# Kernel optimization log

Measured on AMD Instinct MI355X. Metric: run time of the kernel, lower is better.

## Reference

```python
import jax, jax.numpy as jnp
import numpy as np

HID = 15
H = 4
N = 1048576
XD, YD, ZD, TD = 16, 8, 8, 4


def _lin(x, W, b):
    # plain constrained linear (non_negative=False)
    return x @ W.T + b


def _lin_nn(x, W, b):
    # non_negative=True: softplus on the weight before the matmul
    return x @ jax.nn.softplus(W).T + b


def setup_inputs() -> dict:
    key = jax.random.key(0)
    ks = iter(jax.random.split(key, 64))

    def w(shape):
        return jax.random.normal(next(ks), shape, dtype=jnp.float32) * 0.1

    inp = {
        "x0": jax.random.normal(next(ks), (N, XD), dtype=jnp.float32),
        "y0": jax.random.normal(next(ks), (N, YD), dtype=jnp.float32),
        "z0": jax.random.normal(next(ks), (N, ZD), dtype=jnp.float32),
        "t0": jax.random.normal(next(ks), (N, TD), dtype=jnp.float32),
        # y / z / t towers: first layer maps from input dim, rest HIDxHID
        "yW0": w((HID, YD)), "yWs": w((H - 1, HID, HID)), "yb": jnp.zeros((H, HID)),
        "zW0": w((HID, ZD)), "zWs": w((H - 1, HID, HID)), "zb": jnp.zeros((H, HID)),
        "tW0": w((HID, TD)), "tWs": w((H - 1, HID, HID)), "tb": jnp.zeros((H, HID)),
        # first x block (4-branch sum)
        "x0W": w((HID, XD)), "x0b": jnp.zeros((HID,)),
        "y0W": w((HID, YD)), "y0b": jnp.zeros((HID,)),
        "z0W": w((HID, ZD)), "z0b": jnp.zeros((HID,)),
        "t0W": w((HID, TD)), "t0b": jnp.zeros((HID,)),
        # H-1 iterations of 5-branch blocks (stacked along axis 0)
        "xWs": w((H - 1, HID, HID)), "xb": jnp.zeros((H - 1, HID)),
        "xsW": w((H - 1, HID, XD)), "xsb": jnp.zeros((H - 1, HID)),
        "xyW": w((H - 1, HID, HID)), "xyb": jnp.zeros((H - 1, HID)),
        "xzW": w((H - 1, HID, HID)), "xzb": jnp.zeros((H - 1, HID)),
        "xtW": w((H - 1, HID, HID)), "xtb": jnp.zeros((H - 1, HID)),
        "fW": w((HID, HID)), "fb": jnp.zeros((HID,)),
    }
    return inp


def reference(x0, y0, z0, t0,
              yW0, yWs, yb, zW0, zWs, zb, tW0, tWs, tb,
              x0W, x0b, y0W, y0b, z0W, z0b, t0W, t0b,
              xWs, xb, xsW, xsb, xyW, xyb, xzW, xzb, xtW, xtb,
              fW, fb):
    # y tower: softplus activation, non-negative weights
    y = jax.nn.softplus(_lin_nn(y0, yW0, yb[0]))
    for i in range(H - 1):
        y = jax.nn.softplus(_lin_nn(y, yWs[i], yb[i + 1]))
    # z tower: sigmoid activation, unconstrained weights
    z = jax.nn.sigmoid(_lin(z0, zW0, zb[0]))
    for i in range(H - 1):
        z = jax.nn.sigmoid(_lin(z, zWs[i], zb[i + 1]))
    # t tower: sigmoid activation, non-negative weights
    t = jax.nn.sigmoid(_lin_nn(t0, tW0, tb[0]))
    for i in range(H - 1):
        t = jax.nn.sigmoid(_lin_nn(t, tWs[i], tb[i + 1]))
    # x path: multi-branch sums + softplus
    x = _lin(x0, x0W, x0b) + _lin_nn(y0, y0W, y0b) + _lin(z0, z0W, z0b) + _lin_nn(t0, t0W, t0b)
    x = jax.nn.softplus(x)
    for i in range(H - 1):
        x = (_lin_nn(x, xWs[i], xb[i]) + _lin(x0, xsW[i], xsb[i])
             + _lin_nn(y, xyW[i], xyb[i]) + _lin(z, xzW[i], xzb[i])
             + _lin_nn(t, xtW[i], xtb[i]))
        x = jax.nn.softplus(x)
    return _lin(x, fW, fb)
```

## Files before the change

kernel.cpp:

```cpp
#include <hip/hip_runtime.h>
#include <hip/hip_bf16.h>

typedef short s8v  __attribute__((ext_vector_type(8)));
typedef float f32x4 __attribute__((ext_vector_type(4)));
typedef unsigned int u32;
typedef u32 u32x4 __attribute__((ext_vector_type(4)));

#define NSLOT 31
#define NBIAS 17

__device__ __forceinline__ unsigned short b16hi(float v) {
  unsigned int u = __float_as_uint(v);
  return (unsigned short)((u + 0x7FFFu + ((u >> 16) & 1u)) >> 16);
}
__device__ __forceinline__ float b16tof(unsigned short h) {
  return __uint_as_float(((unsigned int)h) << 16);
}
__device__ __forceinline__ unsigned short lobits(float w) {
  return b16hi(w - b16tof(b16hi(w)));
}
__device__ __forceinline__ float sp_stable(float v) {
  float ax = __builtin_fabsf(v);
  float e  = __expf(-ax);
  return fmaxf(v, 0.0f) + __logf(1.0f + e);
}

struct P {
  const float *yW0,*yWs,*yb,*zW0,*zWs,*zb,*tW0,*tWs,*tb;
  const float *x0W,*x0b,*y0W,*y0b,*z0W,*z0b,*t0W,*t0b;
  const float *xWs,*xb,*xsW,*xsb,*xyW,*xyb,*xzW,*xzb,*xtW,*xtb,*fW,*fb;
};

__device__ unsigned short pat15(const float* W, int k, int j, int sp) {
  if (k < 15)           { float v = W[j*15+k];      return b16hi(sp ? sp_stable(v) : v); }
  if (k >= 16 && k < 31){ float v = W[j*15+(k-16)]; return lobits(sp ? sp_stable(v) : v); }
  return 0;
}

__device__ unsigned short wA(int s, int k, int j, const P& p) {
  if (j > 14) return 0;
  if (s == 0) {
    if (k < 8)   return b16hi(sp_stable(p.yW0[j*8+k]));
    if (k < 16)  return lobits(sp_stable(p.yW0[j*8+(k-8)]));
    return 0;
  }
  if (s <= 3)  return pat15(p.yWs + (s-1)*225, k, j, 1);
  if (s == 4) {
    if (k < 8)   return b16hi(p.zW0[j*8+k]);
    if (k < 16)  return lobits(p.zW0[j*8+(k-8)]);
    return 0;
  }
  if (s <= 7)  return pat15(p.zWs + (s-5)*225, k, j, 0);
  if (s == 8) {
    if (k < 4)   return b16hi(sp_stable(p.tW0[j*4+k]));
    if (k < 8)   return lobits(sp_stable(p.tW0[j*4+(k-4)]));
    return 0;
  }
  if (s <= 11) return pat15(p.tWs + (s-9)*225, k, j, 1);
  if (s == 12) {
    if (k < 16) return b16hi(p.x0W[j*16+k]);
    return lobits(p.x0W[j*16+(k-16)]);
  }
  if (s == 13) {
    if (k < 8)  return b16hi(sp_stable(p.y0W[j*8+k]));
    if (k < 16) return b16hi(p.z0W[j*8+(k-8)]);
    if (k < 24) return lobits(sp_stable(p.y0W[j*8+(k-16)]));
    return lobits(p.z0W[j*8+(k-24)]);
  }
  if (s == 14) {
    if (k < 4)  return b16hi(sp_stable(p.t0W[j*4+k]));
    if (k < 8)  return lobits(sp_stable(p.t0W[j*4+(k-4)]));
    return 0;
  }
  if (s <= 29) {
    int i = (s-15)/5, r = (s-15)%5;
    if (r == 0) return pat15(p.xWs + i*225, k, j, 1);
    if (r == 1) {
      const float* W = p.xsW + i*240;
      if (k < 16) return b16hi(W[j*16+k]);
      return lobits(W[j*16+(k-16)]);
    }
    if (r == 2) return pat15(p.xyW + i*225, k, j, 1);
    if (r == 3) return pat15(p.xzW + i*225, k, j, 0);
    return pat15(p.xtW + i*225, k, j, 1);
  }
  return pat15(p.fW, k, j, 0);
}

__global__ void prep_kernel(P p, u32* Abuf, float* biasb) {
  const int tid = blockIdx.x * blockDim.x + threadIdx.x;
  const int str = gridDim.x * blockDim.x;
  for (int idx = tid; idx < NSLOT*256; idx += str) {
    int s = idx >> 8, rem = idx & 255, l = rem >> 2, d = rem & 3;
    int g = l >> 4, j = l & 15;
    int kb = (d < 2) ? (4*g + 2*d) : (16 + 4*g + 2*(d-2));
    u32 v0 = wA(s, kb,   j, p);
    u32 v1 = wA(s, kb+1, j, p);
    Abuf[idx] = v0 | (v1 << 16);
  }
  for (int idx = tid; idx < NBIAS*16; idx += str) {
    int b = idx >> 4, n = idx & 15;
    float v = 0.f;
    if (n < 15) {
      if (b < 4)        v = p.yb[b*15 + n];
      else if (b < 8)   v = p.zb[(b-4)*15 + n];
      else if (b < 12)  v = p.tb[(b-8)*15 + n];
      else if (b == 12) v = p.x0b[n] + p.y0b[n] + p.z0b[n] + p.t0b[n];
      else if (b < 16)  { int i = b - 13;
        v = p.xb[i*15+n] + p.xsb[i*15+n] + p.xyb[i*15+n]
          + p.xzb[i*15+n] + p.xtb[i*15+n]; }
      else              v = p.fb[n];
    }
    biasb[idx] = v;
  }
}

union FragU { u32x4 u; s8v s; };
__device__ __forceinline__ s8v mkfrag(u32 a, u32 b, u32 c, u32 d) {
  FragU f; f.u = u32x4{a, b, c, d}; return f.s;
}
__device__ __forceinline__ u32 pk(float lo, float hi) {
  union { __hip_bfloat162 h; u32 u; } cv;
  cv.h = __float22bfloat162_rn(float2{lo, hi});
  return cv.u;
}
__device__ __forceinline__ float lo16f(u32 u) { return __uint_as_float(u << 16); }
__device__ __forceinline__ float hi16f(u32 u) { return __uint_as_float(u & 0xFFFF0000u); }

#define MFMA(A,B,C) __builtin_amdgcn_mfma_f32_16x16x32_bf16((A),(B),(C),0,0,0)

__device__ __forceinline__ void act_sp(f32x4 a, u32& h0, u32& h1,
                                       u32& l0, u32& l1) {
  const f32x4 z4 = {0.f, 0.f, 0.f, 0.f};
  f32x4 ax = __builtin_elementwise_abs(a);
  f32x4 mx = __builtin_elementwise_max(a, z4);
  f32x4 nt = ax * -1.442695041f;
  f32x4 e;
  e[0] = __builtin_amdgcn_exp2f(nt[0]); e[1] = __builtin_amdgcn_exp2f(nt[1]);
  e[2] = __builtin_amdgcn_exp2f(nt[2]); e[3] = __builtin_amdgcn_exp2f(nt[3]);
  f32x4 op = e + 1.0f;
  f32x4 lg;
  lg[0] = __builtin_amdgcn_logf(op[0]); lg[1] = __builtin_amdgcn_logf(op[1]);
  lg[2] = __builtin_amdgcn_logf(op[2]); lg[3] = __builtin_amdgcn_logf(op[3]);
  f32x4 v = lg * 0.6931471806f + mx;
  h0 = pk(v[0], v[1]);
  h1 = pk(v[2], v[3]);
  l0 = pk(v[0] - lo16f(h0), v[1] - hi16f(h0));
  l1 = pk(v[2] - lo16f(h1), v[3] - hi16f(h1));
}
__device__ __forceinline__ void act_sig(f32x4 a, u32& d0, u32& d1) {
  f32x4 nt = a * -1.442695041f;
  f32x4 e;
  e[0] = __builtin_amdgcn_exp2f(nt[0]); e[1] = __builtin_amdgcn_exp2f(nt[1]);
  e[2] = __builtin_amdgcn_exp2f(nt[2]); e[3] = __builtin_amdgcn_exp2f(nt[3]);
  f32x4 op = e + 1.0f;
  float r0 = __builtin_amdgcn_rcpf(op[0]), r1 = __builtin_amdgcn_rcpf(op[1]);
  float r2 = __builtin_amdgcn_rcpf(op[2]), r3 = __builtin_amdgcn_rcpf(op[3]);
  d0 = pk(r0, r1);
  d1 = pk(r2, r3);
}

#define NWAVE 16

__global__ __launch_bounds__(1024, 8) void isnn_fwd(
    const float* __restrict__ x0g, const float* __restrict__ y0g,
    const float* __restrict__ z0g, const float* __restrict__ t0g,
    const u32* __restrict__ Abuf, const float* __restrict__ biasg,
    float* __restrict__ outg)
{
  __shared__ u32x4 wlds[NSLOT*64];
  __shared__ float blds[NBIAS*16];
  __shared__ float olds[NWAVE][320];

  const int tid = threadIdx.x;
  for (int i = tid; i < NSLOT*64; i += 1024) wlds[i] = ((const u32x4*)Abuf)[i];
  for (int i = tid; i < NBIAS*16; i += 1024) blds[i] = biasg[i];
  __syncthreads();

  const int lane = tid & 63;
  const int w    = tid >> 6;
  const int g    = lane >> 4;
  const int c    = lane & 15;

  const char* wbase = (const char*)wlds + lane * 16;
#define AW(s)   (*(const s8v*)(wbase + (s)*1024))
  const char* bbase = (const char*)blds + g * 16;
#define BIAS(s) (*(const f32x4*)(bbase + (s)*64))

  const int T = blockIdx.x * NWAVE + w;

  float4 x4 = ((const float4*)x0g)[(size_t)(T*16 + c)*4 + g];
  float4 y4 = ((const float4*)y0g)[(size_t)(T*16 + c)*2 + (g & 1)];
  float4 z4 = ((const float4*)z0g)[(size_t)(T*16 + c)*2 + (g & 1)];
  float4 t4 = ((const float4*)t0g)[(size_t)(T*16 + c)];

  u32 dx0 = pk(x4.x, x4.y), dx1 = pk(x4.z, x4.w);
  u32 dy0 = pk(y4.x, y4.y), dy1 = pk(y4.z, y4.w);
  u32 dz0 = pk(z4.x, z4.y), dz1 = pk(z4.z, z4.w);
  u32 dt0 = pk(t4.x, t4.y), dt1 = pk(t4.z, t4.w);
  s8v Bx0 = mkfrag(dx0, dx1, dx0, dx1);
  s8v By0 = mkfrag(dy0, dy1, 0u, 0u);
  s8v Bz0 = mkfrag(dz0, dz1, 0u, 0u);
  s8v Bt0 = mkfrag((g < 2) ? dt0 : 0u, (g < 2) ? dt1 : 0u, 0u, 0u);
  u32 syz0 = (g < 2) ? dy0 : dz0, syz1 = (g < 2) ? dy1 : dz1;
  s8v Byz = mkfrag(syz0, syz1, syz0, syz1);

  f32x4 aY = MFMA(AW(0), By0, BIAS(0));
  f32x4 aZ = MFMA(AW(4), Bz0, BIAS(4));
  f32x4 aT = MFMA(AW(8), Bt0, BIAS(8));

  u32 yh0, yh1, yl0, yl1, zf0, zf1, tf0, tf1;
#pragma unroll
  for (int l = 0; l < 3; ++l) {
    act_sp(aY, yh0, yh1, yl0, yl1);
    act_sig(aZ, zf0, zf1);
    act_sig(aT, tf0, tf1);
    s8v ay = AW(1+l);
    aY = MFMA(ay, mkfrag(yh0, yh1, yh0, yh1), BIAS(1+l));
    aY = MFMA(ay, mkfrag(yl0, yl1, 0u, 0u), aY);
    aZ = MFMA(AW(5+l), mkfrag(zf0, zf1, zf0, zf1), BIAS(5+l));
    aT = MFMA(AW(9+l), mkfrag(tf0, tf1, tf0, tf1), BIAS(9+l));
  }
  act_sp(aY, yh0, yh1, yl0, yl1);
  act_sig(aZ, zf0, zf1);
  act_sig(aT, tf0, tf1);
  s8v FyH = mkfrag(yh0, yh1, yh0, yh1);
  s8v FyL = mkfrag(yl0, yl1, 0u, 0u);
  s8v Fz  = mkfrag(zf0, zf1, zf0, zf1);
  s8v Ft  = mkfrag(tf0, tf1, tf0, tf1);

  f32x4 aX = MFMA(AW(12), Bx0, BIAS(12));
  aX = MFMA(AW(13), Byz, aX);
  aX = MFMA(AW(14), Bt0, aX);

  u32 xh0, xh1, xl0, xl1;
#pragma unroll
  for (int i = 0; i < 3; ++i) {
    act_sp(aX, xh0, xh1, xl0, xl1);
    s8v ax = AW(15+5*i);
    aX = MFMA(ax, mkfrag(xh0, xh1, xh0, xh1), BIAS(13+i));
    aX = MFMA(ax, mkfrag(xl0, xl1, 0u, 0u), aX);
    aX = MFMA(AW(16+5*i), Bx0, aX);
    s8v axy = AW(17+5*i);
    aX = MFMA(axy, FyH, aX);
    aX = MFMA(axy, FyL, aX);
    aX = MFMA(AW(18+5*i), Fz, aX);
    aX = MFMA(AW(19+5*i), Ft, aX);
  }

  act_sp(aX, xh0, xh1, xl0, xl1);
  s8v af = AW(30);
  f32x4 aO = MFMA(af, mkfrag(xh0, xh1, xh0, xh1), BIAS(16));
  aO = MFMA(af, mkfrag(xl0, xl1, 0u, 0u), aO);

  *(f32x4*)(&olds[w][c*20 + 4*g]) = aO;
  float* orow = outg + (size_t)T * 240;
#pragma unroll
  for (int jj = 0; jj < 4; ++jj) {
    int i = lane + 64*jj;
    if (i < 240) {
      int row = i / 15, ch = i - row*15;
      orow[i] = olds[w][row*20 + ch];
    }
  }
#undef AW
#undef BIAS
}

extern "C" void kernel_launch(void* const* d_in, const int* in_sizes, int n_in,
                              void* d_out, int out_size, void* d_ws, size_t ws_size,
                              hipStream_t stream) {
  P p;
  p.yW0 = (const float*)d_in[4];  p.yWs = (const float*)d_in[5];  p.yb  = (const float*)d_in[6];
  p.zW0 = (const float*)d_in[7];  p.zWs = (const float*)d_in[8];  p.zb  = (const float*)d_in[9];
  p.tW0 = (const float*)d_in[10]; p.tWs = (const float*)d_in[11]; p.tb  = (const float*)d_in[12];
  p.x0W = (const float*)d_in[13]; p.x0b = (const float*)d_in[14];
  p.y0W = (const float*)d_in[15]; p.y0b = (const float*)d_in[16];
  p.z0W = (const float*)d_in[17]; p.z0b = (const float*)d_in[18];
  p.t0W = (const float*)d_in[19]; p.t0b = (const float*)d_in[20];
  p.xWs = (const float*)d_in[21]; p.xb  = (const float*)d_in[22];
  p.xsW = (const float*)d_in[23]; p.xsb = (const float*)d_in[24];
  p.xyW = (const float*)d_in[25]; p.xyb = (const float*)d_in[26];
  p.xzW = (const float*)d_in[27]; p.xzb = (const float*)d_in[28];
  p.xtW = (const float*)d_in[29]; p.xtb = (const float*)d_in[30];
  p.fW  = (const float*)d_in[31]; p.fb  = (const float*)d_in[32];

  u32* Abuf = (u32*)d_ws;
  float* biasb = (float*)(Abuf + NSLOT*256);

  prep_kernel<<<8, 256, 0, stream>>>(p, Abuf, biasb);

  const float* x0 = (const float*)d_in[0];
  const float* y0 = (const float*)d_in[1];
  const float* z0 = (const float*)d_in[2];
  const float* t0 = (const float*)d_in[3];

  const int n = in_sizes[0] / 16;
  const int blocks = n / (NWAVE * 16);
  isnn_fwd<<<blocks, 1024, 0, stream>>>(x0, y0, z0, t0, Abuf, biasb, (float*)d_out);
}
```

Before: 110.2 us.

## Process two tiles per wave and prefetch inputs ahead of weight staging

Each wave now handles two 16-row tiles instead of one, so the grid is halved and the cost of staging weights and biases into LDS is spread over twice the work. The first tile's global input loads are issued before the LDS weight copy and barrier, and the second tile's loads are issued before the first tile is computed, so global latency overlaps with the staging and the compute. A scheduling barrier separates the two tile bodies. The trade-off is more live registers and fewer blocks, which can hurt occupancy or tail balance.

```diff
diff --git a/kernel.cpp b/kernel.cpp
--- a/kernel.cpp
+++ b/kernel.cpp
@@ -160,44 +160,29 @@
   d1 = pk(r2, r3);
 }
 
-#define NWAVE 16
-
-__global__ __launch_bounds__(1024, 8) void isnn_fwd(
-    const float* __restrict__ x0g, const float* __restrict__ y0g,
-    const float* __restrict__ z0g, const float* __restrict__ t0g,
-    const u32* __restrict__ Abuf, const float* __restrict__ biasg,
-    float* __restrict__ outg)
-{
-  __shared__ u32x4 wlds[NSLOT*64];
-  __shared__ float blds[NBIAS*16];
-  __shared__ float olds[NWAVE][320];
-
-  const int tid = threadIdx.x;
-  for (int i = tid; i < NSLOT*64; i += 1024) wlds[i] = ((const u32x4*)Abuf)[i];
-  for (int i = tid; i < NBIAS*16; i += 1024) blds[i] = biasg[i];
-  __syncthreads();
-
-  const int lane = tid & 63;
-  const int w    = tid >> 6;
-  const int g    = lane >> 4;
-  const int c    = lane & 15;
-
-  const char* wbase = (const char*)wlds + lane * 16;
+struct Pre { float4 x4, y4, z4, t4; };
+
+__device__ __forceinline__ Pre load_in(const float* x0g, const float* y0g,
+                                       const float* z0g, const float* t0g,
+                                       int T, int c, int g) {
+  Pre p;
+  p.x4 = ((const float4*)x0g)[(size_t)(T*16 + c)*4 + g];
+  p.y4 = ((const float4*)y0g)[(size_t)(T*16 + c)*2 + (g & 1)];
+  p.z4 = ((const float4*)z0g)[(size_t)(T*16 + c)*2 + (g & 1)];
+  p.t4 = ((const float4*)t0g)[(size_t)(T*16 + c)];
+  return p;
+}
+
+__device__ __forceinline__ void tile_body(const Pre& in, int T,
+                                          const char* wbase, const char* bbase,
+                                          float* owave, float* outg,
+                                          int lane, int g, int c) {
 #define AW(s)   (*(const s8v*)(wbase + (s)*1024))
-  const char* bbase = (const char*)blds + g * 16;
 #define BIAS(s) (*(const f32x4*)(bbase + (s)*64))
-
-  const int T = blockIdx.x * NWAVE + w;
-
-  float4 x4 = ((const float4*)x0g)[(size_t)(T*16 + c)*4 + g];
-  float4 y4 = ((const float4*)y0g)[(size_t)(T*16 + c)*2 + (g & 1)];
-  float4 z4 = ((const float4*)z0g)[(size_t)(T*16 + c)*2 + (g & 1)];
-  float4 t4 = ((const float4*)t0g)[(size_t)(T*16 + c)];
-
-  u32 dx0 = pk(x4.x, x4.y), dx1 = pk(x4.z, x4.w);
-  u32 dy0 = pk(y4.x, y4.y), dy1 = pk(y4.z, y4.w);
-  u32 dz0 = pk(z4.x, z4.y), dz1 = pk(z4.z, z4.w);
-  u32 dt0 = pk(t4.x, t4.y), dt1 = pk(t4.z, t4.w);
+  u32 dx0 = pk(in.x4.x, in.x4.y), dx1 = pk(in.x4.z, in.x4.w);
+  u32 dy0 = pk(in.y4.x, in.y4.y), dy1 = pk(in.y4.z, in.y4.w);
+  u32 dz0 = pk(in.z4.x, in.z4.y), dz1 = pk(in.z4.z, in.z4.w);
+  u32 dt0 = pk(in.t4.x, in.t4.y), dt1 = pk(in.t4.z, in.t4.w);
   s8v Bx0 = mkfrag(dx0, dx1, dx0, dx1);
   s8v By0 = mkfrag(dy0, dy1, 0u, 0u);
   s8v Bz0 = mkfrag(dz0, dz1, 0u, 0u);
@@ -253,18 +238,58 @@
   f32x4 aO = MFMA(af, mkfrag(xh0, xh1, xh0, xh1), BIAS(16));
   aO = MFMA(af, mkfrag(xl0, xl1, 0u, 0u), aO);
 
-  *(f32x4*)(&olds[w][c*20 + 4*g]) = aO;
+  *(f32x4*)(owave + c*20 + 4*g) = aO;
   float* orow = outg + (size_t)T * 240;
 #pragma unroll
   for (int jj = 0; jj < 4; ++jj) {
     int i = lane + 64*jj;
     if (i < 240) {
       int row = i / 15, ch = i - row*15;
-      orow[i] = olds[w][row*20 + ch];
+      orow[i] = owave[row*20 + ch];
     }
   }
 #undef AW
 #undef BIAS
+}
+
+#define NWAVE 16
+#define NT 2
+
+__global__ __launch_bounds__(1024, 8) void isnn_fwd(
+    const float* __restrict__ x0g, const float* __restrict__ y0g,
+    const float* __restrict__ z0g, const float* __restrict__ t0g,
+    const u32* __restrict__ Abuf, const float* __restrict__ biasg,
+    float* __restrict__ outg)
+{
+  __shared__ u32x4 wlds[NSLOT*64];
+  __shared__ float blds[NBIAS*16];
+  __shared__ float olds[NWAVE][320];
+
+  const int tid  = threadIdx.x;
+  const int lane = tid & 63;
+  const int w    = tid >> 6;
+  const int g    = lane >> 4;
+  const int c    = lane & 15;
+
+  const int T0 = (blockIdx.x * NWAVE + w) * NT;
+
+  Pre p0 = load_in(x0g, y0g, z0g, t0g, T0, c, g);
+
+  for (int i = tid; i < NSLOT*64; i += 1024) wlds[i] = ((const u32x4*)Abuf)[i];
+  for (int i = tid; i < NBIAS*16; i += 1024) blds[i] = biasg[i];
+  __syncthreads();
+
+  const char* wbase = (const char*)wlds + lane * 16;
+  const char* bbase = (const char*)blds + g * 16;
+  float* owave = &olds[w][0];
+
+  Pre p1 = load_in(x0g, y0g, z0g, t0g, T0 + 1, c, g);
+
+  tile_body(p0, T0, wbase, bbase, owave, outg, lane, g, c);
+
+  __builtin_amdgcn_sched_barrier(0);
+
+  tile_body(p1, T0 + 1, wbase, bbase, owave, outg, lane, g, c);
 }
 
 extern "C" void kernel_launch(void* const* d_in, const int* in_sizes, int n_in,
@@ -296,6 +321,6 @@
   const float* t0 = (const float*)d_in[3];
 
   const int n = in_sizes[0] / 16;
-  const int blocks = n / (NWAVE * 16);
+  const int blocks = n / (NWAVE * 16 * NT);
   isnn_fwd<<<blocks, 1024, 0, stream>>>(x0, y0, z0, t0, Abuf, biasb, (float*)d_out);
 }
```

New measurement: 110.1 us. Within noise of the previous version (-0.1%).
